# Performance work log

Measured on AMD Instinct MI355X. Metric: run time of the kernel, lower is better.

## Reference

```python
import jax, jax.numpy as jnp
import numpy as np

N_NODES = 100000
N_EDGES = 3200000
EMBED = 64
DIMS = [(64, 32), (32, 16)]  # (in_dim, out_dim) per Aggregator layer
EPS = 1e-12


def setup_inputs() -> dict:
    key = jax.random.key(0)
    ks = jax.random.split(key, 16)
    inp = {
        "aux_info_all": jax.random.normal(ks[0], (N_NODES, 3), jnp.float32),
        "entity_embed": jax.random.normal(ks[1], (N_NODES, EMBED), jnp.float32) * 0.1,
        "aux_W": jax.random.normal(ks[2], (EMBED, 3), jnp.float32) * 0.3,
        "aux_b": jnp.zeros((EMBED,), jnp.float32),
        "edge_vals": jax.random.uniform(ks[3], (N_EDGES,), jnp.float32),
        "edge_rows": jax.random.randint(ks[4], (N_EDGES,), 0, N_NODES, jnp.int32),
        "edge_cols": jax.random.randint(ks[5], (N_EDGES,), 0, N_NODES, jnp.int32),
    }
    for li, (din, dout) in enumerate(DIMS):
        s = (2.0 / (din + dout)) ** 0.5  # xavier-ish scale
        inp[f"W1_{li}"] = jax.random.normal(ks[6 + 4 * li], (dout, din), jnp.float32) * s
        inp[f"b1_{li}"] = jnp.zeros((dout,), jnp.float32)
        inp[f"W2_{li}"] = jax.random.normal(ks[7 + 4 * li], (dout, din), jnp.float32) * s
        inp[f"b2_{li}"] = jnp.zeros((dout,), jnp.float32)
    return inp


def _l2norm(x):
    return x / jnp.maximum(jnp.linalg.norm(x, axis=1, keepdims=True), EPS)


def reference(aux_info_all, entity_embed, aux_W, aux_b,
              W1_0, b1_0, W2_0, b2_0, W1_1, b1_1, W2_1, b2_1,
              edge_vals, edge_rows, edge_cols):
    # holographic fusion: entity_embed * (1 + tanh(Linear(aux)))
    aux_vec = jnp.tanh(aux_info_all @ aux_W.T + aux_b)
    ego = entity_embed * (1.0 + aux_vec)  # [N, 64]
    all_embed = [ego]
    layers = [(W1_0, b1_0, W2_0, b2_0), (W1_1, b1_1, W2_1, b2_1)]
    for W1, b1, W2, b2 in layers:
        # sparse A_in @ ego: gather messages over edges, segment-sum by destination row
        msgs = edge_vals[:, None] * ego[edge_cols]  # [E, d]
        side = jax.ops.segment_sum(msgs, edge_rows, num_segments=N_NODES)  # [N, d]
        sum_e = jax.nn.leaky_relu((ego + side) @ W1.T + b1)  # bi-interaction branch 1
        bi_e = jax.nn.leaky_relu((ego * side) @ W2.T + b2)   # bi-interaction branch 2
        ego = sum_e + bi_e  # (dropout p=0 in eval)
        all_embed.append(_l2norm(ego))
    return jnp.concatenate(all_embed, axis=1)  # [N, 64+32+16]
```

## Files before the change

kernel.cpp:

```cpp
#include <hip/hip_runtime.h>
#include <math.h>

#define NN 100000
#define NE 3200000
#define OUTD 112
#define BROWS 512
#define NBUCK 196
#define FILL_CH 8192
#define FILL_B ((NE + FILL_CH - 1) / FILL_CH)
#define BLD1_T 1024
#define SORT_T 512

__device__ inline unsigned short f32_to_bf16(float f) {
    unsigned u = __float_as_uint(f);
    u += 0x7FFFu + ((u >> 16) & 1u);
    return (unsigned short)(u >> 16);
}
__device__ inline float bf16_bits_to_f32(unsigned b) {
    return __uint_as_float(b << 16);
}

__global__ void fuse_ego_kernel(const float* __restrict__ aux_info,
                                const float* __restrict__ entity,
                                const float* __restrict__ aux_W,
                                const float* __restrict__ aux_b,
                                unsigned short* __restrict__ ego0h,
                                float* __restrict__ out) {
    int idx = blockIdx.x * blockDim.x + threadIdx.x;
    if (idx >= NN * 64) return;
    int n = idx >> 6;
    int j = idx & 63;
    float a0 = aux_info[n * 3 + 0];
    float a1 = aux_info[n * 3 + 1];
    float a2 = aux_info[n * 3 + 2];
    float w0 = aux_W[j * 3 + 0];
    float w1 = aux_W[j * 3 + 1];
    float w2 = aux_W[j * 3 + 2];
    float t = tanhf(fmaf(a0, w0, fmaf(a1, w1, fmaf(a2, w2, aux_b[j]))));
    float e = entity[idx] * (1.0f + t);
    ego0h[idx] = f32_to_bf16(e);
    out[(size_t)n * OUTD + j] = e;
}

__global__ void bhist_kernel(const int* __restrict__ rows, int* __restrict__ gcount) {
    __shared__ int h[NBUCK];
    for (int i = threadIdx.x; i < NBUCK; i += BLD1_T) h[i] = 0;
    __syncthreads();
    int base = blockIdx.x * FILL_CH;
    int nE = NE - base; if (nE > FILL_CH) nE = FILL_CH;
    for (int i = threadIdx.x; i < nE; i += BLD1_T)
        atomicAdd(&h[rows[base + i] >> 9], 1);
    __syncthreads();
    for (int i = threadIdx.x; i < NBUCK; i += BLD1_T)
        if (h[i]) atomicAdd(&gcount[i], h[i]);
}

__global__ void bscan_kernel(const int* __restrict__ gcount,
                             int* __restrict__ bucket_base,
                             int* __restrict__ gcursor) {
    __shared__ int sh[256];
    int t = threadIdx.x;
    int v = (t < NBUCK) ? gcount[t] : 0;
    sh[t] = v;
    __syncthreads();
    for (int off = 1; off < 256; off <<= 1) {
        int u = (t >= off) ? sh[t - off] : 0;
        __syncthreads();
        sh[t] += u;
        __syncthreads();
    }
    if (t < NBUCK) {
        int excl = sh[t] - v;
        bucket_base[t] = excl;
        gcursor[t] = excl;
    }
    if (t == 255) bucket_base[NBUCK] = sh[255];
}

__global__ void bucket_fill_kernel(const int* __restrict__ rows,
                                   const int* __restrict__ cols,
                                   const float* __restrict__ vals,
                                   int* __restrict__ gcursor,
                                   int2* __restrict__ edges_b) {
    __shared__ int rowsL[FILL_CH];
    __shared__ int hcnt[NBUCK];
    __shared__ int curs[NBUCK];
    int base = blockIdx.x * FILL_CH;
    int nE = NE - base; if (nE > FILL_CH) nE = FILL_CH;
    for (int i = threadIdx.x; i < NBUCK; i += BLD1_T) hcnt[i] = 0;
    __syncthreads();
    for (int i = threadIdx.x; i < nE; i += BLD1_T) {
        int r = rows[base + i];
        rowsL[i] = r;
        atomicAdd(&hcnt[r >> 9], 1);
    }
    __syncthreads();
    for (int b = threadIdx.x; b < NBUCK; b += BLD1_T) {
        int c = hcnt[b];
        curs[b] = c ? atomicAdd(&gcursor[b], c) : 0;
    }
    __syncthreads();
    for (int i = threadIdx.x; i < nE; i += BLD1_T) {
        int r = rowsL[i];
        int b = r >> 9;
        int p = atomicAdd(&curs[b], 1);
        edges_b[p] = make_int2(cols[base + i] | ((r & (BROWS - 1)) << 17),
                               __float_as_int(vals[base + i]));
    }
}

__global__ void csr_sort_kernel(const int2* __restrict__ edges_b,
                                const int* __restrict__ bucket_base,
                                unsigned int* __restrict__ edges,
                                int* __restrict__ row_ptr) {
    __shared__ int cnt[BROWS];
    __shared__ int scn[BROWS];
    __shared__ int curs[BROWS];
    int b = blockIdx.x;
    int beg = bucket_base[b], end = bucket_base[b + 1];
    int t = threadIdx.x;
    cnt[t] = 0;
    __syncthreads();
    for (int i = beg + t; i < end; i += SORT_T)
        atomicAdd(&cnt[(edges_b[i].x >> 17) & (BROWS - 1)], 1);
    __syncthreads();
    scn[t] = cnt[t];
    __syncthreads();
    for (int off = 1; off < BROWS; off <<= 1) {
        int v = (t >= off) ? scn[t - off] : 0;
        __syncthreads();
        scn[t] += v;
        __syncthreads();
    }
    {
        int excl = scn[t] - cnt[t];
        int n = b * BROWS + t;
        if (n <= NN) row_ptr[n] = beg + excl;
        curs[t] = beg + excl;
    }
    __syncthreads();
    for (int i = beg + t; i < end; i += SORT_T) {
        int2 e = edges_b[i];
        int rl = (e.x >> 17) & (BROWS - 1);
        int p = atomicAdd(&curs[rl], 1);
        unsigned int vb = f32_to_bf16(__int_as_float(e.y)) & 0x7FFFu;
        edges[p] = (unsigned int)(e.x & 0x1FFFF) | (vb << 17);
    }
}

template <int D>
__global__ void gather_kernel(const ushort2* __restrict__ egoh,
                              const unsigned int* __restrict__ edges,
                              const int* __restrict__ row_ptr,
                              float* __restrict__ side) {
    constexpr int L = D / 2;
    int n = blockIdx.x * (256 / L) + threadIdx.x / L;
    int j = threadIdx.x % L;
    if (n >= NN) return;
    int beg = row_ptr[n];
    int end = row_ptr[n + 1];
    float a0 = 0.0f, a1 = 0.0f;
    int i = beg;
    for (; i + 8 <= end; i += 8) {
        unsigned int e[8];
        ushort2 gv[8];
#pragma unroll
        for (int k = 0; k < 8; ++k) e[k] = edges[i + k];
#pragma unroll
        for (int k = 0; k < 8; ++k) gv[k] = egoh[(size_t)(e[k] & 0x1FFFFu) * L + j];
#pragma unroll
        for (int k = 0; k < 8; ++k) {
            float v = bf16_bits_to_f32(e[k] >> 17);
            a0 = fmaf(v, bf16_bits_to_f32(gv[k].x), a0);
            a1 = fmaf(v, bf16_bits_to_f32(gv[k].y), a1);
        }
    }
    for (; i < end; ++i) {
        unsigned int e = edges[i];
        ushort2 g = egoh[(size_t)(e & 0x1FFFFu) * L + j];
        float v = bf16_bits_to_f32(e >> 17);
        a0 = fmaf(v, bf16_bits_to_f32(g.x), a0);
        a1 = fmaf(v, bf16_bits_to_f32(g.y), a1);
    }
    side[(size_t)n * D + 2 * j]     = a0;
    side[(size_t)n * D + 2 * j + 1] = a1;
}

template <int DIN, int DOUT, int NB>
__global__ void layer_kernel(const float* __restrict__ ego, int ego_stride,
                             const float* __restrict__ side,
                             const float* __restrict__ W1,
                             const float* __restrict__ b1,
                             const float* __restrict__ W2,
                             const float* __restrict__ b2,
                             float* __restrict__ ego_next,
                             unsigned short* __restrict__ ego_next_h,
                             float* __restrict__ out,
                             int out_off) {
    __shared__ float W1t[DIN][DOUT + 1];
    __shared__ float W2t[DIN][DOUT + 1];
    __shared__ float egoL[NB][DIN];
    __shared__ float sideL[NB][DIN];

    for (int i = threadIdx.x; i < DIN * DOUT; i += blockDim.x) {
        int j = i / DIN;
        int k = i - j * DIN;
        W1t[k][j] = W1[i];
        W2t[k][j] = W2[i];
    }
    int node0 = blockIdx.x * NB;
    for (int i = threadIdx.x; i < NB * DIN; i += blockDim.x) {
        int m = i / DIN;
        int k = i - m * DIN;
        int n = node0 + m;
        if (n < NN) {
            egoL[m][k] = ego[(size_t)n * ego_stride + k];
            sideL[m][k] = side[(size_t)n * DIN + k];
        }
    }
    __syncthreads();

    int m = threadIdx.x / DOUT;
    int j = threadIdx.x % DOUT;
    int n = node0 + m;
    if (n >= NN) return;

    float s = b1[j];
    float bb = b2[j];
#pragma unroll
    for (int k = 0; k < DIN; ++k) {
        float eg = egoL[m][k];
        float sd = sideL[m][k];
        s = fmaf(eg + sd, W1t[k][j], s);
        bb = fmaf(eg * sd, W2t[k][j], bb);
    }
    s = (s > 0.0f) ? s : 0.01f * s;
    bb = (bb > 0.0f) ? bb : 0.01f * bb;
    float v = s + bb;
    if (ego_next)   ego_next[(size_t)n * DOUT + j] = v;
    if (ego_next_h) ego_next_h[(size_t)n * DOUT + j] = f32_to_bf16(v);

    float sq = v * v;
#pragma unroll
    for (int off = DOUT / 2; off > 0; off >>= 1)
        sq += __shfl_xor(sq, off, DOUT);
    float norm = sqrtf(sq);
    norm = (norm > 1e-12f) ? norm : 1e-12f;
    out[(size_t)n * OUTD + out_off + j] = v / norm;
}

extern "C" void kernel_launch(void* const* d_in, const int* in_sizes, int n_in,
                              void* d_out, int out_size, void* d_ws, size_t ws_size,
                              hipStream_t stream) {
    const float* aux_info  = (const float*)d_in[0];
    const float* entity    = (const float*)d_in[1];
    const float* aux_W     = (const float*)d_in[2];
    const float* aux_b     = (const float*)d_in[3];
    const float* edge_vals = (const float*)d_in[4];
    const int*   edge_rows = (const int*)d_in[5];
    const int*   edge_cols = (const int*)d_in[6];
    const float* W1_0 = (const float*)d_in[7];
    const float* b1_0 = (const float*)d_in[8];
    const float* W2_0 = (const float*)d_in[9];
    const float* b2_0 = (const float*)d_in[10];
    const float* W1_1 = (const float*)d_in[11];
    const float* b1_1 = (const float*)d_in[12];
    const float* W2_1 = (const float*)d_in[13];
    const float* b2_1 = (const float*)d_in[14];
    float* out = (float*)d_out;

    float* region0 = (float*)d_ws;
    int2*  edges_b = (int2*)region0;
    float* side0   = region0;
    unsigned short* ego0h = (unsigned short*)(region0 + (size_t)NE * 2);
    unsigned short* ego1h = ego0h;
    unsigned int* edges = (unsigned int*)((float*)ego0h + (size_t)NN * 32);
    float* ego1  = (float*)(edges + NE);
    float* side1 = ego1 + (size_t)NN * 32;
    int* row_ptr     = (int*)(side1 + (size_t)NN * 32);
    int* bucket_base = row_ptr + NN + 1;
    int* gcount      = bucket_base + NBUCK + 1;

    hipMemsetAsync(gcount, 0, (size_t)NBUCK * sizeof(int), stream);
    bhist_kernel<<<FILL_B, BLD1_T, 0, stream>>>(edge_rows, gcount);
    bscan_kernel<<<1, 256, 0, stream>>>(gcount, bucket_base, gcount);
    bucket_fill_kernel<<<FILL_B, BLD1_T, 0, stream>>>(
        edge_rows, edge_cols, edge_vals, gcount, edges_b);
    csr_sort_kernel<<<NBUCK, SORT_T, 0, stream>>>(edges_b, bucket_base, edges, row_ptr);

    {
        int total = NN * 64;
        fuse_ego_kernel<<<(total + 255) / 256, 256, 0, stream>>>(
            aux_info, entity, aux_W, aux_b, ego0h, out);
    }
    gather_kernel<64><<<(NN + 7) / 8, 256, 0, stream>>>(
        (const ushort2*)ego0h, edges, row_ptr, side0);
    layer_kernel<64, 32, 8><<<(NN + 7) / 8, 256, 0, stream>>>(
        out, OUTD, side0, W1_0, b1_0, W2_0, b2_0, ego1, ego1h, out, 64);
    gather_kernel<32><<<(NN + 15) / 16, 256, 0, stream>>>(
        (const ushort2*)ego1h, edges, row_ptr, side1);
    layer_kernel<32, 16, 16><<<(NN + 15) / 16, 256, 0, stream>>>(
        ego1, 32, side1, W1_1, b1_1, W2_1, b2_1, nullptr, nullptr, out, 96);
}
```

Before: 413.7 us.

## Fuse sparse gather with bi-interaction layer transform in one kernel

Merges the per-layer SpMM gather kernel and the dense bi-interaction/normalize kernel into a single kernel. Each block gathers neighbor sums for its nodes, forms ego+side and ego*side directly into shared memory, then applies the two small linear layers, so the side buffer no longer round-trips through global memory and two launches are removed. The workspace layout changes so ego1h no longer aliases ego0h. The grid uses NN/8 and NN/16 blocks with no bounds check, which relies on NN dividing evenly.

```diff
diff --git a/kernel.cpp b/kernel.cpp
--- a/kernel.cpp
+++ b/kernel.cpp
@@ -148,97 +148,95 @@
     }
 }
 
-template <int D>
-__global__ void gather_kernel(const ushort2* __restrict__ egoh,
-                              const unsigned int* __restrict__ edges,
-                              const int* __restrict__ row_ptr,
-                              float* __restrict__ side) {
-    constexpr int L = D / 2;
-    int n = blockIdx.x * (256 / L) + threadIdx.x / L;
-    int j = threadIdx.x % L;
-    if (n >= NN) return;
-    int beg = row_ptr[n];
-    int end = row_ptr[n + 1];
-    float a0 = 0.0f, a1 = 0.0f;
-    int i = beg;
-    for (; i + 8 <= end; i += 8) {
-        unsigned int e[8];
-        ushort2 gv[8];
-#pragma unroll
-        for (int k = 0; k < 8; ++k) e[k] = edges[i + k];
-#pragma unroll
-        for (int k = 0; k < 8; ++k) gv[k] = egoh[(size_t)(e[k] & 0x1FFFFu) * L + j];
-#pragma unroll
-        for (int k = 0; k < 8; ++k) {
-            float v = bf16_bits_to_f32(e[k] >> 17);
-            a0 = fmaf(v, bf16_bits_to_f32(gv[k].x), a0);
-            a1 = fmaf(v, bf16_bits_to_f32(gv[k].y), a1);
-        }
-    }
-    for (; i < end; ++i) {
-        unsigned int e = edges[i];
-        ushort2 g = egoh[(size_t)(e & 0x1FFFFu) * L + j];
-        float v = bf16_bits_to_f32(e >> 17);
-        a0 = fmaf(v, bf16_bits_to_f32(g.x), a0);
-        a1 = fmaf(v, bf16_bits_to_f32(g.y), a1);
-    }
-    side[(size_t)n * D + 2 * j]     = a0;
-    side[(size_t)n * D + 2 * j + 1] = a1;
-}
-
-template <int DIN, int DOUT, int NB>
-__global__ void layer_kernel(const float* __restrict__ ego, int ego_stride,
-                             const float* __restrict__ side,
-                             const float* __restrict__ W1,
-                             const float* __restrict__ b1,
-                             const float* __restrict__ W2,
-                             const float* __restrict__ b2,
-                             float* __restrict__ ego_next,
-                             unsigned short* __restrict__ ego_next_h,
-                             float* __restrict__ out,
-                             int out_off) {
+template <int DIN, int DOUT>
+__global__ __launch_bounds__(256) void fused_gather_layer_kernel(
+    const ushort2* __restrict__ egoh,
+    const unsigned int* __restrict__ edges,
+    const int* __restrict__ row_ptr,
+    const float* __restrict__ ego, int ego_stride,
+    const float* __restrict__ W1, const float* __restrict__ b1,
+    const float* __restrict__ W2, const float* __restrict__ b2,
+    float* __restrict__ ego_next,
+    unsigned short* __restrict__ ego_next_h,
+    float* __restrict__ out, int out_off)
+{
+    constexpr int L  = DIN / 2;
+    constexpr int NB = 256 / L;
+    static_assert(L == DOUT, "gather/transform lane mapping must coincide");
+
     __shared__ float W1t[DIN][DOUT + 1];
     __shared__ float W2t[DIN][DOUT + 1];
-    __shared__ float egoL[NB][DIN];
-    __shared__ float sideL[NB][DIN];
-
-    for (int i = threadIdx.x; i < DIN * DOUT; i += blockDim.x) {
-        int j = i / DIN;
-        int k = i - j * DIN;
-        W1t[k][j] = W1[i];
-        W2t[k][j] = W2[i];
-    }
-    int node0 = blockIdx.x * NB;
-    for (int i = threadIdx.x; i < NB * DIN; i += blockDim.x) {
-        int m = i / DIN;
-        int k = i - m * DIN;
-        int n = node0 + m;
-        if (n < NN) {
-            egoL[m][k] = ego[(size_t)n * ego_stride + k];
-            sideL[m][k] = side[(size_t)n * DIN + k];
+    __shared__ float sArr[NB][DIN + 4];
+    __shared__ float pArr[NB][DIN + 4];
+
+    for (int i = threadIdx.x; i < DIN * DOUT; i += 256) {
+        int jj = i / DIN;
+        int kk = i - jj * DIN;
+        W1t[kk][jj] = W1[i];
+        W2t[kk][jj] = W2[i];
+    }
+
+    const int m = threadIdx.x / L;
+    const int j = threadIdx.x % L;
+    const int n = blockIdx.x * NB + m;
+
+    {
+        int beg = row_ptr[n];
+        int end = row_ptr[n + 1];
+        float a0 = 0.0f, a1 = 0.0f;
+        int i = beg;
+        for (; i + 8 <= end; i += 8) {
+            unsigned int e[8];
+            ushort2 gv[8];
+#pragma unroll
+            for (int k = 0; k < 8; ++k) e[k] = edges[i + k];
+#pragma unroll
+            for (int k = 0; k < 8; ++k) gv[k] = egoh[(size_t)(e[k] & 0x1FFFFu) * L + j];
+#pragma unroll
+            for (int k = 0; k < 8; ++k) {
+                float v = bf16_bits_to_f32(e[k] >> 17);
+                a0 = fmaf(v, bf16_bits_to_f32(gv[k].x), a0);
+                a1 = fmaf(v, bf16_bits_to_f32(gv[k].y), a1);
+            }
         }
-    }
-    __syncthreads();
-
-    int m = threadIdx.x / DOUT;
-    int j = threadIdx.x % DOUT;
-    int n = node0 + m;
-    if (n >= NN) return;
-
-    float s = b1[j];
-    float bb = b2[j];
-#pragma unroll
-    for (int k = 0; k < DIN; ++k) {
-        float eg = egoL[m][k];
-        float sd = sideL[m][k];
-        s = fmaf(eg + sd, W1t[k][j], s);
-        bb = fmaf(eg * sd, W2t[k][j], bb);
-    }
-    s = (s > 0.0f) ? s : 0.01f * s;
+        for (; i < end; ++i) {
+            unsigned int e = edges[i];
+            ushort2 g = egoh[(size_t)(e & 0x1FFFFu) * L + j];
+            float v = bf16_bits_to_f32(e >> 17);
+            a0 = fmaf(v, bf16_bits_to_f32(g.x), a0);
+            a1 = fmaf(v, bf16_bits_to_f32(g.y), a1);
+        }
+        float e0 = ego[(size_t)n * ego_stride + 2 * j];
+        float e1 = ego[(size_t)n * ego_stride + 2 * j + 1];
+        *(float2*)&sArr[m][2 * j] = make_float2(e0 + a0, e1 + a1);
+        *(float2*)&pArr[m][2 * j] = make_float2(e0 * a0, e1 * a1);
+    }
+    __syncthreads();
+
+    const int mt = threadIdx.x / DOUT;
+    const int jt = threadIdx.x % DOUT;
+    const int nt = blockIdx.x * NB + mt;
+
+    float s  = b1[jt];
+    float bb = b2[jt];
+#pragma unroll
+    for (int k = 0; k < DIN; k += 4) {
+        float4 sv = *(const float4*)&sArr[mt][k];
+        float4 pv = *(const float4*)&pArr[mt][k];
+        s  = fmaf(sv.x, W1t[k + 0][jt], s);
+        s  = fmaf(sv.y, W1t[k + 1][jt], s);
+        s  = fmaf(sv.z, W1t[k + 2][jt], s);
+        s  = fmaf(sv.w, W1t[k + 3][jt], s);
+        bb = fmaf(pv.x, W2t[k + 0][jt], bb);
+        bb = fmaf(pv.y, W2t[k + 1][jt], bb);
+        bb = fmaf(pv.z, W2t[k + 2][jt], bb);
+        bb = fmaf(pv.w, W2t[k + 3][jt], bb);
+    }
+    s  = (s  > 0.0f) ? s  : 0.01f * s;
     bb = (bb > 0.0f) ? bb : 0.01f * bb;
     float v = s + bb;
-    if (ego_next)   ego_next[(size_t)n * DOUT + j] = v;
-    if (ego_next_h) ego_next_h[(size_t)n * DOUT + j] = f32_to_bf16(v);
+    if (ego_next)   ego_next[(size_t)nt * DOUT + jt] = v;
+    if (ego_next_h) ego_next_h[(size_t)nt * DOUT + jt] = f32_to_bf16(v);
 
     float sq = v * v;
 #pragma unroll
@@ -246,7 +244,7 @@
         sq += __shfl_xor(sq, off, DOUT);
     float norm = sqrtf(sq);
     norm = (norm > 1e-12f) ? norm : 1e-12f;
-    out[(size_t)n * OUTD + out_off + j] = v / norm;
+    out[(size_t)nt * OUTD + out_off + jt] = v / norm;
 }
 
 extern "C" void kernel_launch(void* const* d_in, const int* in_sizes, int n_in,
@@ -271,13 +269,11 @@
 
     float* region0 = (float*)d_ws;
     int2*  edges_b = (int2*)region0;
-    float* side0   = region0;
     unsigned short* ego0h = (unsigned short*)(region0 + (size_t)NE * 2);
-    unsigned short* ego1h = ego0h;
     unsigned int* edges = (unsigned int*)((float*)ego0h + (size_t)NN * 32);
-    float* ego1  = (float*)(edges + NE);
-    float* side1 = ego1 + (size_t)NN * 32;
-    int* row_ptr     = (int*)(side1 + (size_t)NN * 32);
+    float* ego1 = (float*)(edges + NE);
+    unsigned short* ego1h = (unsigned short*)(ego1 + (size_t)NN * 32);
+    int* row_ptr     = (int*)((float*)ego1h + (size_t)NN * 16);
     int* bucket_base = row_ptr + NN + 1;
     int* gcount      = bucket_base + NBUCK + 1;
 
@@ -293,12 +289,10 @@
         fuse_ego_kernel<<<(total + 255) / 256, 256, 0, stream>>>(
             aux_info, entity, aux_W, aux_b, ego0h, out);
     }
-    gather_kernel<64><<<(NN + 7) / 8, 256, 0, stream>>>(
-        (const ushort2*)ego0h, edges, row_ptr, side0);
-    layer_kernel<64, 32, 8><<<(NN + 7) / 8, 256, 0, stream>>>(
-        out, OUTD, side0, W1_0, b1_0, W2_0, b2_0, ego1, ego1h, out, 64);
-    gather_kernel<32><<<(NN + 15) / 16, 256, 0, stream>>>(
-        (const ushort2*)ego1h, edges, row_ptr, side1);
-    layer_kernel<32, 16, 16><<<(NN + 15) / 16, 256, 0, stream>>>(
-        ego1, 32, side1, W1_1, b1_1, W2_1, b2_1, nullptr, nullptr, out, 96);
-}
+    fused_gather_layer_kernel<64, 32><<<NN / 8, 256, 0, stream>>>(
+        (const ushort2*)ego0h, edges, row_ptr, out, OUTD,
+        W1_0, b1_0, W2_0, b2_0, ego1, ego1h, out, 64);
+    fused_gather_layer_kernel<32, 16><<<NN / 16, 256, 0, stream>>>(
+        (const ushort2*)ego1h, edges, row_ptr, ego1, 32,
+        W1_1, b1_1, W2_1, b2_1, nullptr, nullptr, out, 96);
+}
```

Measured after the change: 459.9 us. 1.11x slower.

## Register-tile layer kernel over 64 nodes per block and unroll gather by 16

Applied to the files above, without the earlier changes.

The layer kernel now precomputes ego+side and ego*side into shared memory with float4 loads. Each thread keeps accumulators for several nodes and reads weights straight from global memory as float4, replacing the per-block shared-memory weight transpose. Blocks handle 64 nodes instead of 8 or 16, so weight staging is amortized and there are fewer blocks. The gather kernel also gets a 16-wide unrolled loop for more memory-level parallelism, at the cost of higher register pressure.

```diff
diff --git a/kernel.cpp b/kernel.cpp
--- a/kernel.cpp
+++ b/kernel.cpp
@@ -161,6 +161,20 @@
     int end = row_ptr[n + 1];
     float a0 = 0.0f, a1 = 0.0f;
     int i = beg;
+    for (; i + 16 <= end; i += 16) {
+        unsigned int e[16];
+        ushort2 gv[16];
+#pragma unroll
+        for (int k = 0; k < 16; ++k) e[k] = edges[i + k];
+#pragma unroll
+        for (int k = 0; k < 16; ++k) gv[k] = egoh[(size_t)(e[k] & 0x1FFFFu) * L + j];
+#pragma unroll
+        for (int k = 0; k < 16; ++k) {
+            float v = bf16_bits_to_f32(e[k] >> 17);
+            a0 = fmaf(v, bf16_bits_to_f32(gv[k].x), a0);
+            a1 = fmaf(v, bf16_bits_to_f32(gv[k].y), a1);
+        }
+    }
     for (; i + 8 <= end; i += 8) {
         unsigned int e[8];
         ushort2 gv[8];
@@ -187,66 +201,86 @@
 }
 
 template <int DIN, int DOUT, int NB>
-__global__ void layer_kernel(const float* __restrict__ ego, int ego_stride,
-                             const float* __restrict__ side,
-                             const float* __restrict__ W1,
-                             const float* __restrict__ b1,
-                             const float* __restrict__ W2,
-                             const float* __restrict__ b2,
-                             float* __restrict__ ego_next,
-                             unsigned short* __restrict__ ego_next_h,
-                             float* __restrict__ out,
-                             int out_off) {
-    __shared__ float W1t[DIN][DOUT + 1];
-    __shared__ float W2t[DIN][DOUT + 1];
-    __shared__ float egoL[NB][DIN];
-    __shared__ float sideL[NB][DIN];
-
-    for (int i = threadIdx.x; i < DIN * DOUT; i += blockDim.x) {
-        int j = i / DIN;
-        int k = i - j * DIN;
-        W1t[k][j] = W1[i];
-        W2t[k][j] = W2[i];
-    }
-    int node0 = blockIdx.x * NB;
-    for (int i = threadIdx.x; i < NB * DIN; i += blockDim.x) {
-        int m = i / DIN;
-        int k = i - m * DIN;
+__global__ __launch_bounds__(256) void layer_kernel(
+    const float* __restrict__ ego, int ego_stride,
+    const float* __restrict__ side,
+    const float* __restrict__ W1, const float* __restrict__ b1,
+    const float* __restrict__ W2, const float* __restrict__ b2,
+    float* __restrict__ ego_next,
+    unsigned short* __restrict__ ego_next_h,
+    float* __restrict__ out, int out_off)
+{
+    constexpr int RW  = DIN + 4;
+    constexpr int CH  = DIN / 4;
+    constexpr int NPT = NB * DOUT / 256;
+    static_assert(NB * DOUT % 256 == 0, "");
+
+    __shared__ float sArr[NB][RW];
+    __shared__ float pArr[NB][RW];
+
+    const int node0 = blockIdx.x * NB;
+
+    for (int i = threadIdx.x; i < NB * CH; i += 256) {
+        int m = i / CH;
+        int c = i - m * CH;
         int n = node0 + m;
         if (n < NN) {
-            egoL[m][k] = ego[(size_t)n * ego_stride + k];
-            sideL[m][k] = side[(size_t)n * DIN + k];
-        }
-    }
-    __syncthreads();
-
-    int m = threadIdx.x / DOUT;
-    int j = threadIdx.x % DOUT;
-    int n = node0 + m;
-    if (n >= NN) return;
-
-    float s = b1[j];
-    float bb = b2[j];
-#pragma unroll
-    for (int k = 0; k < DIN; ++k) {
-        float eg = egoL[m][k];
-        float sd = sideL[m][k];
-        s = fmaf(eg + sd, W1t[k][j], s);
-        bb = fmaf(eg * sd, W2t[k][j], bb);
-    }
-    s = (s > 0.0f) ? s : 0.01f * s;
-    bb = (bb > 0.0f) ? bb : 0.01f * bb;
-    float v = s + bb;
-    if (ego_next)   ego_next[(size_t)n * DOUT + j] = v;
-    if (ego_next_h) ego_next_h[(size_t)n * DOUT + j] = f32_to_bf16(v);
-
-    float sq = v * v;
-#pragma unroll
-    for (int off = DOUT / 2; off > 0; off >>= 1)
-        sq += __shfl_xor(sq, off, DOUT);
-    float norm = sqrtf(sq);
-    norm = (norm > 1e-12f) ? norm : 1e-12f;
-    out[(size_t)n * OUTD + out_off + j] = v / norm;
+            float4 e  = *(const float4*)&ego[(size_t)n * ego_stride + c * 4];
+            float4 sd = *(const float4*)&side[(size_t)n * DIN + c * 4];
+            *(float4*)&sArr[m][c * 4] =
+                make_float4(e.x + sd.x, e.y + sd.y, e.z + sd.z, e.w + sd.w);
+            *(float4*)&pArr[m][c * 4] =
+                make_float4(e.x * sd.x, e.y * sd.y, e.z * sd.z, e.w * sd.w);
+        }
+    }
+    __syncthreads();
+
+    const int j    = threadIdx.x % DOUT;
+    const int slot = threadIdx.x / DOUT;
+
+    float acc1[NPT], acc2[NPT];
+    float bb1 = b1[j], bb2 = b2[j];
+#pragma unroll
+    for (int m8 = 0; m8 < NPT; ++m8) { acc1[m8] = bb1; acc2[m8] = bb2; }
+
+#pragma unroll
+    for (int kg = 0; kg < CH; ++kg) {
+        float4 w1 = *(const float4*)&W1[j * DIN + kg * 4];
+        float4 w2 = *(const float4*)&W2[j * DIN + kg * 4];
+#pragma unroll
+        for (int m8 = 0; m8 < NPT; ++m8) {
+            int m = slot * NPT + m8;
+            float4 sv = *(const float4*)&sArr[m][kg * 4];
+            float4 pv = *(const float4*)&pArr[m][kg * 4];
+            acc1[m8] = fmaf(sv.x, w1.x, acc1[m8]);
+            acc1[m8] = fmaf(sv.y, w1.y, acc1[m8]);
+            acc1[m8] = fmaf(sv.z, w1.z, acc1[m8]);
+            acc1[m8] = fmaf(sv.w, w1.w, acc1[m8]);
+            acc2[m8] = fmaf(pv.x, w2.x, acc2[m8]);
+            acc2[m8] = fmaf(pv.y, w2.y, acc2[m8]);
+            acc2[m8] = fmaf(pv.z, w2.z, acc2[m8]);
+            acc2[m8] = fmaf(pv.w, w2.w, acc2[m8]);
+        }
+    }
+
+#pragma unroll
+    for (int m8 = 0; m8 < NPT; ++m8) {
+        int n = node0 + slot * NPT + m8;
+        float s  = acc1[m8]; s  = (s  > 0.0f) ? s  : 0.01f * s;
+        float bb = acc2[m8]; bb = (bb > 0.0f) ? bb : 0.01f * bb;
+        float v = s + bb;
+        float sq = v * v;
+#pragma unroll
+        for (int off = DOUT / 2; off > 0; off >>= 1)
+            sq += __shfl_xor(sq, off, DOUT);
+        float norm = sqrtf(sq);
+        norm = (norm > 1e-12f) ? norm : 1e-12f;
+        if (n < NN) {
+            if (ego_next)   ego_next[(size_t)n * DOUT + j] = v;
+            if (ego_next_h) ego_next_h[(size_t)n * DOUT + j] = f32_to_bf16(v);
+            out[(size_t)n * OUTD + out_off + j] = v / norm;
+        }
+    }
 }
 
 extern "C" void kernel_launch(void* const* d_in, const int* in_sizes, int n_in,
@@ -295,10 +329,10 @@
     }
     gather_kernel<64><<<(NN + 7) / 8, 256, 0, stream>>>(
         (const ushort2*)ego0h, edges, row_ptr, side0);
-    layer_kernel<64, 32, 8><<<(NN + 7) / 8, 256, 0, stream>>>(
+    layer_kernel<64, 32, 64><<<(NN + 63) / 64, 256, 0, stream>>>(
         out, OUTD, side0, W1_0, b1_0, W2_0, b2_0, ego1, ego1h, out, 64);
     gather_kernel<32><<<(NN + 15) / 16, 256, 0, stream>>>(
         (const ushort2*)ego1h, edges, row_ptr, side1);
-    layer_kernel<32, 16, 16><<<(NN + 15) / 16, 256, 0, stream>>>(
+    layer_kernel<32, 16, 64><<<(NN + 63) / 64, 256, 0, stream>>>(
         ego1, 32, side1, W1_1, b1_1, W2_1, b2_1, nullptr, nullptr, out, 96);
 }
```

Result: slower. 843.7 us (+103.9%).
